# Optimization experiments

Measured on AMD Instinct MI355X. Metric: run time of the kernel, lower is better.

The kernel has to match this reference:

```python
import jax, jax.numpy as jnp
import numpy as np

N = 100000      # nodes
E = 1600000     # edges (avg degree 16)
DIN = 128
DH = 128
DOUT = 64
K = 2           # SGConv propagation steps
EPS = 1e-5      # BatchNorm eps


def setup_inputs() -> dict:
    key = jax.random.key(0)
    ks = jax.random.split(key, 12)
    x = jax.random.normal(ks[0], (N, DIN), dtype=jnp.float32)
    edge_index = jax.random.randint(ks[1], (2, E), 0, N, dtype=jnp.int32)
    def lin(k, fin, fout):
        k1, k2 = jax.random.split(k)
        s = 1.0 / np.sqrt(fin)
        W = jax.random.uniform(k1, (fin, fout), jnp.float32, -s, s)
        b = jax.random.uniform(k2, (fout,), jnp.float32, -s, s)
        return W, b
    W1, b1 = lin(ks[2], DIN, DH)
    W2, b2 = lin(ks[3], DH, DH)
    W3, b3 = lin(ks[4], DH, DOUT)
    g1 = jnp.ones((DH,), jnp.float32); be1 = jnp.zeros((DH,), jnp.float32)
    g2 = jnp.ones((DH,), jnp.float32); be2 = jnp.zeros((DH,), jnp.float32)
    return {"x": x, "edge_index": edge_index,
            "W1": W1, "b1": b1, "g1": g1, "be1": be1,
            "W2": W2, "b2": b2, "g2": g2, "be2": be2,
            "W3": W3, "b3": b3}


def _sgc_propagate(h, row, col, norm):
    # h: [N, d]; gather source nodes, scale per-edge, scatter-add to dest
    for _ in range(K):
        msg = norm[:, None] * h[row]                      # [E, d]
        h = jax.ops.segment_sum(msg, col, num_segments=N)  # [N, d]
    return h


def _batchnorm(h, gamma, beta):
    # training-mode BN over node axis, biased variance (torch semantics)
    mu = jnp.mean(h, axis=0)
    var = jnp.mean(jnp.square(h - mu), axis=0)
    return gamma * (h - mu) * jax.lax.rsqrt(var + EPS) + beta


def reference(x, edge_index, W1, b1, g1, be1, W2, b2, g2, be2, W3, b3):
    row, col = edge_index[0], edge_index[1]
    # symmetric degree normalization; degree counted on row (as in source)
    deg = jax.ops.segment_sum(jnp.ones((E,), x.dtype), row, num_segments=N)
    dis = jnp.where(deg > 0, 1.0 / jnp.sqrt(jnp.maximum(deg, 1.0)), 0.0)
    norm = dis[row] * dis[col]                             # [E]

    h = _sgc_propagate(x, row, col, norm)
    h = _batchnorm(h @ W1 + b1, g1, be1)   # dropout p=0.0 -> identity
    h = _sgc_propagate(h, row, col, norm)
    h = _batchnorm(h @ W2 + b2, g2, be2)
    return h @ W3 + b3                      # [N, DOUT]
```

## Files before the change

kernel.cpp:

```cpp
#include <hip/hip_runtime.h>


typedef __attribute__((ext_vector_type(8))) short bf16x8;
typedef __attribute__((ext_vector_type(4))) float f32x4;

#define HR_RBITS 14
#define HR_RSIZE 16384
#define HR_NRANGE 7
#define HR_NCHUNK 100
#define HR_WPC (HR_NRANGE * HR_RSIZE / 2)

#define PA_NCHUNK 256
#define PB_SHIFT 8

static inline size_t align256(size_t x) { return (x + 255) & ~(size_t)255; }

__device__ inline unsigned short bf16rn(float f) {
    unsigned int u = __builtin_bit_cast(unsigned int, f);
    u += 0x7fffu + ((u >> 16) & 1u);
    return (unsigned short)(u >> 16);
}
__device__ inline float bflo(unsigned int u) { return __builtin_bit_cast(float, u << 16); }
__device__ inline float bfhi(unsigned int u) { return __builtin_bit_cast(float, u & 0xffff0000u); }
__device__ inline unsigned int packbf2(float a, float b) {
    return (unsigned int)bf16rn(a) | ((unsigned int)bf16rn(b) << 16);
}

__global__ void hist_row_kernel(const int* __restrict__ row, int E,
                                unsigned int* __restrict__ staging) {
    __shared__ unsigned int l32[HR_RSIZE / 2];
    int range = blockIdx.x % HR_NRANGE;
    int chunk = blockIdx.x / HR_NRANGE;
    for (int i = threadIdx.x; i < HR_RSIZE / 2; i += 256) l32[i] = 0;
    __syncthreads();
    int lo = range << HR_RBITS;
    int ebeg = (int)((long long)E * chunk / HR_NCHUNK);
    int eend = (int)((long long)E * (chunk + 1) / HR_NCHUNK);
    for (int i = ebeg + threadIdx.x * 4; i + 3 < eend; i += 256 * 4) {
        int4 v = *(const int4*)(row + i);
        unsigned a;
        a = (unsigned)(v.x - lo); if (a < HR_RSIZE) atomicAdd(&l32[a >> 1], (a & 1) ? 0x10000u : 1u);
        a = (unsigned)(v.y - lo); if (a < HR_RSIZE) atomicAdd(&l32[a >> 1], (a & 1) ? 0x10000u : 1u);
        a = (unsigned)(v.z - lo); if (a < HR_RSIZE) atomicAdd(&l32[a >> 1], (a & 1) ? 0x10000u : 1u);
        a = (unsigned)(v.w - lo); if (a < HR_RSIZE) atomicAdd(&l32[a >> 1], (a & 1) ? 0x10000u : 1u);
    }
    __syncthreads();
    unsigned int* dst = staging + (size_t)chunk * HR_WPC + (lo >> 1);
    for (int i = threadIdx.x; i < HR_RSIZE / 2; i += 256) dst[i] = l32[i];
}

__global__ void dis_kernel(const unsigned int* __restrict__ staging, float* __restrict__ dis, int n) {
    int i = blockIdx.x * blockDim.x + threadIdx.x;
    if (i < n) {
        int shift = (i & 1) * 16;
        int d = 0;
#pragma unroll 4
        for (int c = 0; c < HR_NCHUNK; ++c)
            d += (staging[(size_t)c * HR_WPC + (i >> 1)] >> shift) & 0xffff;
        dis[i] = d > 0 ? rsqrtf((float)d) : 0.f;
    }
}


__global__ void pa_hist_kernel(const int* __restrict__ col, int E,
                               int* __restrict__ chunkhist, int nbuck) {
    __shared__ int lh[512];
    int chunk = blockIdx.x;
    for (int i = threadIdx.x; i < nbuck; i += 256) lh[i] = 0;
    __syncthreads();
    int ebeg = (int)((long long)E * chunk / PA_NCHUNK);
    int eend = (int)((long long)E * (chunk + 1) / PA_NCHUNK);
    for (int i = ebeg + threadIdx.x; i < eend; i += 256)
        atomicAdd(&lh[col[i] >> PB_SHIFT], 1);
    __syncthreads();
    for (int i = threadIdx.x; i < nbuck; i += 256)
        chunkhist[i * PA_NCHUNK + chunk] = lh[i];
}

__global__ void pa_scan1_kernel(int* __restrict__ chunkhist, int* __restrict__ tot) {
    __shared__ int sh[PA_NCHUNK];
    int b = blockIdx.x, t = threadIdx.x;
    int* p = chunkhist + b * PA_NCHUNK;
    int v = p[t];
    sh[t] = v;
    __syncthreads();
    for (int off = 1; off < PA_NCHUNK; off <<= 1) {
        int tv = (t >= off) ? sh[t - off] : 0;
        __syncthreads();
        sh[t] += tv;
        __syncthreads();
    }
    p[t] = sh[t] - v;
    if (t == PA_NCHUNK - 1) tot[b] = sh[t];
}

__global__ void pa_scan2_kernel(const int* __restrict__ tot, int* __restrict__ bucketstart,
                                int nbuck) {
    __shared__ int sh[512];
    int t = threadIdx.x;
    int v = (t < nbuck) ? tot[t] : 0;
    sh[t] = v;
    __syncthreads();
    for (int off = 1; off < 512; off <<= 1) {
        int tv = (t >= off) ? sh[t - off] : 0;
        __syncthreads();
        sh[t] += tv;
        __syncthreads();
    }
    if (t < nbuck) bucketstart[t] = sh[t] - v;
    if (t == 511) bucketstart[nbuck] = sh[511];
}

__global__ void pa_scatter_kernel(const int* __restrict__ row, const int* __restrict__ col,
                                  int E, const int* __restrict__ chunkhist,
                                  const int* __restrict__ bucketstart,
                                  int2* __restrict__ part, int nbuck) {
    __shared__ int loff[512];
    int chunk = blockIdx.x;
    for (int i = threadIdx.x; i < nbuck; i += 256)
        loff[i] = chunkhist[i * PA_NCHUNK + chunk] + bucketstart[i];
    __syncthreads();
    int ebeg = (int)((long long)E * chunk / PA_NCHUNK);
    int eend = (int)((long long)E * (chunk + 1) / PA_NCHUNK);
    for (int i = ebeg + threadIdx.x; i < eend; i += 256) {
        int r = row[i], c = col[i];
        int pos = atomicAdd(&loff[c >> PB_SHIFT], 1);
        int2 v; v.x = r; v.y = c;
        part[pos] = v;
    }
}

__global__ void pb_kernel(const int2* __restrict__ part, const int* __restrict__ bucketstart,
                          const float* __restrict__ dis, int2* __restrict__ csr,
                          int* __restrict__ csr_ptr, int n) {
    __shared__ int lcnt[256], sh[256], loff[256];
    int b = blockIdx.x, t = threadIdx.x;
    int nlo = b << PB_SHIFT;
    int ebeg = bucketstart[b], eend = bucketstart[b + 1];
    lcnt[t] = 0;
    __syncthreads();
    for (int i = ebeg + t; i < eend; i += 256)
        atomicAdd(&lcnt[part[i].y - nlo], 1);
    __syncthreads();
    int v = lcnt[t];
    sh[t] = v;
    __syncthreads();
    for (int off = 1; off < 256; off <<= 1) {
        int tv = (t >= off) ? sh[t - off] : 0;
        __syncthreads();
        sh[t] += tv;
        __syncthreads();
    }
    int excl = sh[t] - v;
    loff[t] = excl;
    if (nlo + t <= n) csr_ptr[nlo + t] = ebeg + excl;
    __syncthreads();
    for (int i = ebeg + t; i < eend; i += 256) {
        int2 e = part[i];
        int c = e.y;
        int slot = atomicAdd(&loff[c - nlo], 1);
        int2 o;
        o.x = e.x;
        o.y = __float_as_int(dis[e.x] * dis[c]);
        csr[ebeg + slot] = o;
    }
}


__global__ void xcvt_kernel(const float* __restrict__ x, unsigned int* __restrict__ x16, int total4) {
    for (int i = blockIdx.x * blockDim.x + threadIdx.x; i < total4; i += gridDim.x * blockDim.x) {
        float4 f = ((const float4*)x)[i];
        x16[i * 2] = packbf2(f.x, f.y);
        x16[i * 2 + 1] = packbf2(f.z, f.w);
    }
}

__global__ void wcvt_kernel(const float* __restrict__ W1, const float* __restrict__ W2,
                            unsigned short* __restrict__ W1t, unsigned short* __restrict__ W2t) {
    int i = blockIdx.x * blockDim.x + threadIdx.x;
    if (i < 32768) {
        const float* W = (i < 16384) ? W1 : W2;
        unsigned short* T = (i < 16384) ? W1t : W2t;
        int j = i & 16383;
        int k = j >> 7, c = j & 127;
        T[c * 128 + k] = bf16rn(W[j]);
    }
}


template <bool AFF>
__global__ void spmm16_kernel(const int* __restrict__ csr_ptr, const int2* __restrict__ csr,
                              const unsigned short* __restrict__ h_in,
                              const float* __restrict__ scale, const float* __restrict__ shift,
                              unsigned short* __restrict__ h_out, int n) {
    int gw = __builtin_amdgcn_readfirstlane((blockIdx.x * blockDim.x + threadIdx.x) >> 6);
    int lane = threadIdx.x & 63;
    int sub = lane & 15;
    int grp = lane >> 4;
    if (gw >= n) return;
    uint4* outp = (uint4*)(h_out + (size_t)gw * 128) + sub;
    int beg = csr_ptr[gw];
    int end = csr_ptr[gw + 1];
    int cnt = end - beg;
    if (cnt == 0) {
        if (lane < 16) {
            uint4 z = {0u, 0u, 0u, 0u};
            *outp = z;
        }
        return;
    }
    const int2* base = csr + beg;
    float acc[8];
#pragma unroll
    for (int j = 0; j < 8; ++j) acc[j] = 0.f;
    float sc[8], sh[8];
    if (AFF) {
        float4 s0 = ((const float4*)scale)[sub * 2];
        float4 s1 = ((const float4*)scale)[sub * 2 + 1];
        float4 h0 = ((const float4*)shift)[sub * 2];
        float4 h1 = ((const float4*)shift)[sub * 2 + 1];
        sc[0] = s0.x; sc[1] = s0.y; sc[2] = s0.z; sc[3] = s0.w;
        sc[4] = s1.x; sc[5] = s1.y; sc[6] = s1.z; sc[7] = s1.w;
        sh[0] = h0.x; sh[1] = h0.y; sh[2] = h0.z; sh[3] = h0.w;
        sh[4] = h1.x; sh[5] = h1.y; sh[6] = h1.z; sh[7] = h1.w;
    }
    bool g1 = (grp & 1) != 0;
    bool g2 = (grp & 2) != 0;
    for (int j0 = 0; j0 < cnt; j0 += 16) {
        int2 ent[16];
#pragma unroll
        for (int k = 0; k < 16; ++k) ent[k] = base[j0 + k];
        uint4 u[4];
        float wsel[4];
#pragma unroll
        for (int k = 0; k < 4; ++k) {
            int i0 = j0 + 4 * k;
            int e0 = (i0 + 0 < cnt) ? ent[4 * k + 0].x : 0;
            int e1 = (i0 + 1 < cnt) ? ent[4 * k + 1].x : 0;
            int e2 = (i0 + 2 < cnt) ? ent[4 * k + 2].x : 0;
            int e3 = (i0 + 3 < cnt) ? ent[4 * k + 3].x : 0;
            float w0 = (i0 + 0 < cnt) ? __int_as_float(ent[4 * k + 0].y) : 0.f;
            float w1 = (i0 + 1 < cnt) ? __int_as_float(ent[4 * k + 1].y) : 0.f;
            float w2 = (i0 + 2 < cnt) ? __int_as_float(ent[4 * k + 2].y) : 0.f;
            float w3 = (i0 + 3 < cnt) ? __int_as_float(ent[4 * k + 3].y) : 0.f;
            int eA = g1 ? e1 : e0;
            int eB = g1 ? e3 : e2;
            int esel = g2 ? eB : eA;
            float wA = g1 ? w1 : w0;
            float wB = g1 ? w3 : w2;
            wsel[k] = g2 ? wB : wA;
            u[k] = *(const uint4*)(h_in + (size_t)esel * 128 + sub * 8);
        }
#pragma unroll
        for (int k = 0; k < 4; ++k) {
            float w = wsel[k];
            unsigned int uu[4] = {u[k].x, u[k].y, u[k].z, u[k].w};
#pragma unroll
            for (int q = 0; q < 4; ++q) {
                float f0 = bflo(uu[q]), f1 = bfhi(uu[q]);
                if (AFF) {
                    f0 = fmaf(sc[2 * q], f0, sh[2 * q]);
                    f1 = fmaf(sc[2 * q + 1], f1, sh[2 * q + 1]);
                }
                acc[2 * q] = fmaf(w, f0, acc[2 * q]);
                acc[2 * q + 1] = fmaf(w, f1, acc[2 * q + 1]);
            }
        }
    }
#pragma unroll
    for (int j = 0; j < 8; ++j) {
        acc[j] += __shfl_xor(acc[j], 16, 64);
        acc[j] += __shfl_xor(acc[j], 32, 64);
    }
    if (lane < 16) {
        uint4 o;
        o.x = packbf2(acc[0], acc[1]);
        o.y = packbf2(acc[2], acc[3]);
        o.z = packbf2(acc[4], acc[5]);
        o.w = packbf2(acc[6], acc[7]);
        *outp = o;
    }
}


template <int NCT, bool OUTF32, bool STATS>
__launch_bounds__(256)
__global__ void gemm16_kernel(const unsigned short* __restrict__ X,
                              const unsigned short* __restrict__ Wt,
                              const float* __restrict__ bias, void* __restrict__ Y,
                              float* __restrict__ gsum, float* __restrict__ gsq, int n) {
    __shared__ __align__(16) char lds[NCT * 16 * 256];
    __shared__ float ssum[NCT * 16], ssq[NCT * 16];
    for (int i = threadIdx.x; i < NCT * 16 * 16; i += 256) {
        int col = i >> 4;
        int kbyte = (i & 15) << 4;
        *(uint4*)(lds + col * 256 + (kbyte ^ ((col & 7) << 4))) = ((const uint4*)Wt)[i];
    }
    if (STATS) {
        for (int i = threadIdx.x; i < NCT * 16; i += 256) {
            ssum[i] = 0.f;
            ssq[i] = 0.f;
        }
    }
    __syncthreads();

    int lane = threadIdx.x & 63;
    int wave = threadIdx.x >> 6;
    int cl = lane & 15, g = lane >> 4;

    bf16x8 b[NCT][4];
#pragma unroll
    for (int ct = 0; ct < NCT; ++ct) {
        int col = ct * 16 + cl;
#pragma unroll
        for (int kc = 0; kc < 4; ++kc) {
            int kbyte = kc * 64 + g * 16;
            b[ct][kc] = *(const bf16x8*)(lds + col * 256 + (kbyte ^ ((col & 7) << 4)));
        }
    }
    float bc[NCT];
#pragma unroll
    for (int ct = 0; ct < NCT; ++ct) bc[ct] = bias[ct * 16 + cl];

    for (int rb0 = blockIdx.x * 64; rb0 < n; rb0 += gridDim.x * 64) {
        int rb = rb0 + wave * 16;
        if (rb >= n) continue;
        int row = rb + cl;
        int rowc = row < n ? row : n - 1;
        const unsigned short* xr = X + (size_t)rowc * 128;
        bf16x8 a[4];
#pragma unroll
        for (int kc = 0; kc < 4; ++kc) a[kc] = *(const bf16x8*)(xr + kc * 32 + g * 8);
#pragma unroll
        for (int ct = 0; ct < NCT; ++ct) {
            f32x4 acc = {bc[ct], bc[ct], bc[ct], bc[ct]};
#pragma unroll
            for (int kc = 0; kc < 4; ++kc)
                acc = __builtin_amdgcn_mfma_f32_16x16x32_bf16(a[kc], b[ct][kc], acc, 0, 0, 0);
            int colo = ct * 16 + cl;
            if (STATS) {
                float s = acc[0] + acc[1] + acc[2] + acc[3];
                float q = acc[0] * acc[0] + acc[1] * acc[1] + acc[2] * acc[2] + acc[3] * acc[3];
                s += __shfl_xor(s, 16, 64);
                s += __shfl_xor(s, 32, 64);
                q += __shfl_xor(q, 16, 64);
                q += __shfl_xor(q, 32, 64);
                if (g == 0) {
                    atomicAdd(&ssum[colo], s);
                    atomicAdd(&ssq[colo], q);
                }
            }
#pragma unroll
            for (int i = 0; i < 4; ++i) {
                int ro = rb + g * 4 + i;
                if (ro < n) {
                    if (OUTF32)
                        ((float*)Y)[(size_t)ro * (NCT * 16) + colo] = acc[i];
                    else
                        ((unsigned short*)Y)[(size_t)ro * 128 + colo] = bf16rn(acc[i]);
                }
            }
        }
    }
    if (STATS) {
        __syncthreads();
        for (int i = threadIdx.x; i < NCT * 16; i += 256) {
            atomicAdd(&gsum[i], ssum[i]);
            atomicAdd(&gsq[i], ssq[i]);
        }
    }
}


__global__ void bn_final_kernel(const float* __restrict__ gsum, const float* __restrict__ gsq,
                                const float* __restrict__ gamma, const float* __restrict__ beta,
                                int n, float* __restrict__ scale, float* __restrict__ shift) {
    int c = threadIdx.x;
    if (c < 128) {
        float fn = (float)n;
        float mu = gsum[c] / fn;
        float var = gsq[c] / fn - mu * mu;
        float inv = rsqrtf(var + 1e-5f);
        float sc = gamma[c] * inv;
        scale[c] = sc;
        shift[c] = beta[c] - sc * mu;
    }
}

__global__ void fold_w3_kernel(const float* __restrict__ W3, const float* __restrict__ b3,
                               const float* __restrict__ scale, const float* __restrict__ shift,
                               unsigned short* __restrict__ W3t, float* __restrict__ b3f) {
    int c = threadIdx.x;
    if (c < 64) {
        float acc = b3[c];
        for (int k = 0; k < 128; ++k) {
            float w = W3[k * 64 + c];
            W3t[c * 128 + k] = bf16rn(scale[k] * w);
            acc += shift[k] * w;
        }
        b3f[c] = acc;
    }
}


extern "C" void kernel_launch(void* const* d_in, const int* in_sizes, int n_in,
                              void* d_out, int out_size, void* d_ws, size_t ws_size,
                              hipStream_t stream) {
    const float* x = (const float*)d_in[0];
    const int* edge = (const int*)d_in[1];
    const float* W1 = (const float*)d_in[2];
    const float* b1 = (const float*)d_in[3];
    const float* g1 = (const float*)d_in[4];
    const float* be1 = (const float*)d_in[5];
    const float* W2 = (const float*)d_in[6];
    const float* b2 = (const float*)d_in[7];
    const float* g2 = (const float*)d_in[8];
    const float* be2 = (const float*)d_in[9];
    const float* W3 = (const float*)d_in[10];
    const float* b3 = (const float*)d_in[11];
    float* out = (float*)d_out;

    const int N = in_sizes[0] / 128;
    const int E = in_sizes[1] / 2;
    const int* erow = edge;
    const int* ecol = edge + E;
    const int nbuck = (N + 255) >> PB_SHIFT;

    char* p = (char*)d_ws;
    size_t off = 0;
    auto carve = [&](size_t bytes) {
        void* r = p + off;
        off += align256(bytes);
        return r;
    };
    unsigned short* x16 = (unsigned short*)carve((size_t)N * 128 * 2);
    unsigned short* A16 = (unsigned short*)carve((size_t)N * 128 * 2);
    unsigned short* B16 = (unsigned short*)carve((size_t)N * 128 * 2);
    int2* part = (int2*)carve((size_t)E * 8);
    int2* csr = (int2*)carve((size_t)E * 8 + 256);
    int* csr_ptr = (int*)carve((size_t)(N + 1) * 4);
    int* chunkhist = (int*)carve((size_t)(nbuck + 1) * PA_NCHUNK * 4);
    int* bucketstart = (int*)carve((size_t)(nbuck + 1) * 4);
    int* tot = (int*)carve((size_t)(nbuck + 1) * 4);
    float* dis = (float*)carve((size_t)N * 4);
    float* gsum = (float*)carve(1024);
    float* gsq = (float*)(gsum + 128);
    float* scale1 = (float*)carve(512);
    float* shift1 = (float*)carve(512);
    float* scale2 = (float*)carve(512);
    float* shift2 = (float*)carve(512);
    unsigned short* W1t = (unsigned short*)carve(128 * 128 * 2);
    unsigned short* W2t = (unsigned short*)carve(128 * 128 * 2);
    unsigned short* W3t = (unsigned short*)carve(64 * 128 * 2);
    float* b3f = (float*)carve(256);
    unsigned int* staging = (unsigned int*)part;
    (void)ws_size;

    const int TB = 256;
    const int gN = (N + TB - 1) / TB;
    const int gSp = (N + 3) / 4;
    const int gGemm = (N + 63) / 64;
    const int gGemmS = 320;

    hist_row_kernel<<<HR_NRANGE * HR_NCHUNK, TB, 0, stream>>>(erow, E, staging);
    dis_kernel<<<gN, TB, 0, stream>>>(staging, dis, N);
    pa_hist_kernel<<<PA_NCHUNK, TB, 0, stream>>>(ecol, E, chunkhist, nbuck);
    pa_scan1_kernel<<<nbuck, PA_NCHUNK, 0, stream>>>(chunkhist, tot);
    pa_scan2_kernel<<<1, 512, 0, stream>>>(tot, bucketstart, nbuck);
    pa_scatter_kernel<<<PA_NCHUNK, TB, 0, stream>>>(erow, ecol, E, chunkhist, bucketstart, part, nbuck);
    pb_kernel<<<nbuck, TB, 0, stream>>>(part, bucketstart, dis, csr, csr_ptr, N);

    xcvt_kernel<<<2048, TB, 0, stream>>>(x, (unsigned int*)x16, N * 32);
    wcvt_kernel<<<128, TB, 0, stream>>>(W1, W2, W1t, W2t);

    spmm16_kernel<false><<<gSp, TB, 0, stream>>>(csr_ptr, csr, x16, nullptr, nullptr, A16, N);
    spmm16_kernel<false><<<gSp, TB, 0, stream>>>(csr_ptr, csr, A16, nullptr, nullptr, B16, N);

    hipMemsetAsync(gsum, 0, 1024, stream);
    gemm16_kernel<8, false, true><<<gGemmS, TB, 0, stream>>>(B16, W1t, b1, A16, gsum, gsq, N);
    bn_final_kernel<<<1, 128, 0, stream>>>(gsum, gsq, g1, be1, N, scale1, shift1);

    spmm16_kernel<true><<<gSp, TB, 0, stream>>>(csr_ptr, csr, A16, scale1, shift1, B16, N);
    spmm16_kernel<false><<<gSp, TB, 0, stream>>>(csr_ptr, csr, B16, nullptr, nullptr, A16, N);

    hipMemsetAsync(gsum, 0, 1024, stream);
    gemm16_kernel<8, false, true><<<gGemmS, TB, 0, stream>>>(A16, W2t, b2, B16, gsum, gsq, N);
    bn_final_kernel<<<1, 128, 0, stream>>>(gsum, gsq, g2, be2, N, scale2, shift2);

    fold_w3_kernel<<<1, 64, 0, stream>>>(W3, b3, scale2, shift2, W3t, b3f);
    gemm16_kernel<4, true, false><<<gGemm, TB, 0, stream>>>(B16, W3t, b3f, out, nullptr, nullptr, N);
}
```

Baseline: 400.4 us.

## Switch intermediates to fp16, use dot2 in SpMM and fold BN affine post-aggregation

Intermediate features, weights and edge norms move from bf16 to fp16. The SpMM inner loop now packs two edges' values and weights and uses v_dot2_f32_f16, halving FMA count. The BatchNorm affine is no longer applied per gathered element; it is applied once after aggregation as scale*acc + shift*sum(w). The histogram also gets larger ranges and fewer chunks and now handles a tail of edges. fp16 has less exponent range than bf16, so large intermediate values could overflow.

```diff
diff --git a/kernel.cpp b/kernel.cpp
--- a/kernel.cpp
+++ b/kernel.cpp
@@ -1,13 +1,14 @@
 #include <hip/hip_runtime.h>
-
-
-typedef __attribute__((ext_vector_type(8))) short bf16x8;
+#include <hip/hip_fp16.h>
+
+
+typedef _Float16 f16x8 __attribute__((ext_vector_type(8)));
 typedef __attribute__((ext_vector_type(4))) float f32x4;
 
-#define HR_RBITS 14
-#define HR_RSIZE 16384
-#define HR_NRANGE 7
-#define HR_NCHUNK 100
+#define HR_RBITS 15
+#define HR_RSIZE 32768
+#define HR_NRANGE 4
+#define HR_NCHUNK 96
 #define HR_WPC (HR_NRANGE * HR_RSIZE / 2)
 
 #define PA_NCHUNK 256
@@ -15,15 +16,13 @@
 
 static inline size_t align256(size_t x) { return (x + 255) & ~(size_t)255; }
 
-__device__ inline unsigned short bf16rn(float f) {
-    unsigned int u = __builtin_bit_cast(unsigned int, f);
-    u += 0x7fffu + ((u >> 16) & 1u);
-    return (unsigned short)(u >> 16);
-}
-__device__ inline float bflo(unsigned int u) { return __builtin_bit_cast(float, u << 16); }
-__device__ inline float bfhi(unsigned int u) { return __builtin_bit_cast(float, u & 0xffff0000u); }
-__device__ inline unsigned int packbf2(float a, float b) {
-    return (unsigned int)bf16rn(a) | ((unsigned int)bf16rn(b) << 16);
+__device__ inline unsigned int packh2(float a, float b) {
+    return (unsigned int)__half_as_ushort(__float2half(a)) |
+           ((unsigned int)__half_as_ushort(__float2half(b)) << 16);
+}
+
+__device__ inline void dot2h(float& acc, unsigned int a, unsigned int b) {
+    asm("v_dot2_f32_f16 %0, %1, %2, %0" : "+v"(acc) : "v"(a), "v"(b));
 }
 
 __global__ void hist_row_kernel(const int* __restrict__ row, int E,
@@ -34,8 +33,9 @@
     for (int i = threadIdx.x; i < HR_RSIZE / 2; i += 256) l32[i] = 0;
     __syncthreads();
     int lo = range << HR_RBITS;
-    int ebeg = (int)((long long)E * chunk / HR_NCHUNK);
-    int eend = (int)((long long)E * (chunk + 1) / HR_NCHUNK);
+    int q4 = E >> 2;
+    int ebeg = (int)(((long long)q4 * chunk / HR_NCHUNK) << 2);
+    int eend = (int)(((long long)q4 * (chunk + 1) / HR_NCHUNK) << 2);
     for (int i = ebeg + threadIdx.x * 4; i + 3 < eend; i += 256 * 4) {
         int4 v = *(const int4*)(row + i);
         unsigned a;
@@ -43,6 +43,12 @@
         a = (unsigned)(v.y - lo); if (a < HR_RSIZE) atomicAdd(&l32[a >> 1], (a & 1) ? 0x10000u : 1u);
         a = (unsigned)(v.z - lo); if (a < HR_RSIZE) atomicAdd(&l32[a >> 1], (a & 1) ? 0x10000u : 1u);
         a = (unsigned)(v.w - lo); if (a < HR_RSIZE) atomicAdd(&l32[a >> 1], (a & 1) ? 0x10000u : 1u);
+    }
+    if (chunk == HR_NCHUNK - 1) {
+        for (int i = (E & ~3) + threadIdx.x; i < E; i += 256) {
+            unsigned a = (unsigned)(row[i] - lo);
+            if (a < HR_RSIZE) atomicAdd(&l32[a >> 1], (a & 1) ? 0x10000u : 1u);
+        }
     }
     __syncthreads();
     unsigned int* dst = staging + (size_t)chunk * HR_WPC + (lo >> 1);
@@ -159,9 +165,10 @@
         int2 e = part[i];
         int c = e.y;
         int slot = atomicAdd(&loff[c - nlo], 1);
+        float nrm = dis[e.x] * dis[c];
         int2 o;
         o.x = e.x;
-        o.y = __float_as_int(dis[e.x] * dis[c]);
+        o.y = (int)((unsigned int)__half_as_ushort(__float2half(nrm)) << 16);
         csr[ebeg + slot] = o;
     }
 }
@@ -170,8 +177,8 @@
 __global__ void xcvt_kernel(const float* __restrict__ x, unsigned int* __restrict__ x16, int total4) {
     for (int i = blockIdx.x * blockDim.x + threadIdx.x; i < total4; i += gridDim.x * blockDim.x) {
         float4 f = ((const float4*)x)[i];
-        x16[i * 2] = packbf2(f.x, f.y);
-        x16[i * 2 + 1] = packbf2(f.z, f.w);
+        x16[i * 2] = packh2(f.x, f.y);
+        x16[i * 2 + 1] = packh2(f.z, f.w);
     }
 }
 
@@ -183,7 +190,7 @@
         unsigned short* T = (i < 16384) ? W1t : W2t;
         int j = i & 16383;
         int k = j >> 7, c = j & 127;
-        T[c * 128 + k] = bf16rn(W[j]);
+        T[c * 128 + k] = __half_as_ushort(__float2half(W[j]));
     }
 }
 
@@ -213,17 +220,8 @@
     float acc[8];
 #pragma unroll
     for (int j = 0; j < 8; ++j) acc[j] = 0.f;
-    float sc[8], sh[8];
-    if (AFF) {
-        float4 s0 = ((const float4*)scale)[sub * 2];
-        float4 s1 = ((const float4*)scale)[sub * 2 + 1];
-        float4 h0 = ((const float4*)shift)[sub * 2];
-        float4 h1 = ((const float4*)shift)[sub * 2 + 1];
-        sc[0] = s0.x; sc[1] = s0.y; sc[2] = s0.z; sc[3] = s0.w;
-        sc[4] = s1.x; sc[5] = s1.y; sc[6] = s1.z; sc[7] = s1.w;
-        sh[0] = h0.x; sh[1] = h0.y; sh[2] = h0.z; sh[3] = h0.w;
-        sh[4] = h1.x; sh[5] = h1.y; sh[6] = h1.z; sh[7] = h1.w;
-    }
+    float wsum = 0.f;
+    const unsigned int ones2 = 0x3C003C00u;
     bool g1 = (grp & 1) != 0;
     bool g2 = (grp & 2) != 0;
     for (int j0 = 0; j0 < cnt; j0 += 16) {
@@ -252,18 +250,20 @@
             u[k] = *(const uint4*)(h_in + (size_t)esel * 128 + sub * 8);
         }
 #pragma unroll
-        for (int k = 0; k < 4; ++k) {
-            float w = wsel[k];
-            unsigned int uu[4] = {u[k].x, u[k].y, u[k].z, u[k].w};
+        for (int p = 0; p < 2; ++p) {
+            unsigned int wa = __float_as_uint(wsel[2 * p]);
+            unsigned int wb = __float_as_uint(wsel[2 * p + 1]);
+            unsigned int wp = __builtin_amdgcn_perm(wb, wa, 0x07060302u);
+            if (AFF) dot2h(wsum, ones2, wp);
+            uint4 ua4 = u[2 * p], ub4 = u[2 * p + 1];
+            unsigned int uaw[4] = {ua4.x, ua4.y, ua4.z, ua4.w};
+            unsigned int ubw[4] = {ub4.x, ub4.y, ub4.z, ub4.w};
 #pragma unroll
             for (int q = 0; q < 4; ++q) {
-                float f0 = bflo(uu[q]), f1 = bfhi(uu[q]);
-                if (AFF) {
-                    f0 = fmaf(sc[2 * q], f0, sh[2 * q]);
-                    f1 = fmaf(sc[2 * q + 1], f1, sh[2 * q + 1]);
-                }
-                acc[2 * q] = fmaf(w, f0, acc[2 * q]);
-                acc[2 * q + 1] = fmaf(w, f1, acc[2 * q + 1]);
+                unsigned int lop = __builtin_amdgcn_perm(ubw[q], uaw[q], 0x05040100u);
+                unsigned int hip = __builtin_amdgcn_perm(ubw[q], uaw[q], 0x07060302u);
+                dot2h(acc[2 * q], lop, wp);
+                dot2h(acc[2 * q + 1], hip, wp);
             }
         }
     }
@@ -272,12 +272,28 @@
         acc[j] += __shfl_xor(acc[j], 16, 64);
         acc[j] += __shfl_xor(acc[j], 32, 64);
     }
+    if (AFF) {
+        wsum += __shfl_xor(wsum, 16, 64);
+        wsum += __shfl_xor(wsum, 32, 64);
+        float4 s0 = ((const float4*)scale)[sub * 2];
+        float4 s1 = ((const float4*)scale)[sub * 2 + 1];
+        float4 h0 = ((const float4*)shift)[sub * 2];
+        float4 h1 = ((const float4*)shift)[sub * 2 + 1];
+        acc[0] = fmaf(h0.x, wsum, s0.x * acc[0]);
+        acc[1] = fmaf(h0.y, wsum, s0.y * acc[1]);
+        acc[2] = fmaf(h0.z, wsum, s0.z * acc[2]);
+        acc[3] = fmaf(h0.w, wsum, s0.w * acc[3]);
+        acc[4] = fmaf(h1.x, wsum, s1.x * acc[4]);
+        acc[5] = fmaf(h1.y, wsum, s1.y * acc[5]);
+        acc[6] = fmaf(h1.z, wsum, s1.z * acc[6]);
+        acc[7] = fmaf(h1.w, wsum, s1.w * acc[7]);
+    }
     if (lane < 16) {
         uint4 o;
-        o.x = packbf2(acc[0], acc[1]);
-        o.y = packbf2(acc[2], acc[3]);
-        o.z = packbf2(acc[4], acc[5]);
-        o.w = packbf2(acc[6], acc[7]);
+        o.x = packh2(acc[0], acc[1]);
+        o.y = packh2(acc[2], acc[3]);
+        o.z = packh2(acc[4], acc[5]);
+        o.w = packh2(acc[6], acc[7]);
         *outp = o;
     }
 }
@@ -308,14 +324,14 @@
     int wave = threadIdx.x >> 6;
     int cl = lane & 15, g = lane >> 4;
 
-    bf16x8 b[NCT][4];
+    f16x8 b[NCT][4];
 #pragma unroll
     for (int ct = 0; ct < NCT; ++ct) {
         int col = ct * 16 + cl;
 #pragma unroll
         for (int kc = 0; kc < 4; ++kc) {
             int kbyte = kc * 64 + g * 16;
-            b[ct][kc] = *(const bf16x8*)(lds + col * 256 + (kbyte ^ ((col & 7) << 4)));
+            b[ct][kc] = *(const f16x8*)(lds + col * 256 + (kbyte ^ ((col & 7) << 4)));
         }
     }
     float bc[NCT];
@@ -328,15 +344,15 @@
         int row = rb + cl;
         int rowc = row < n ? row : n - 1;
         const unsigned short* xr = X + (size_t)rowc * 128;
-        bf16x8 a[4];
-#pragma unroll
-        for (int kc = 0; kc < 4; ++kc) a[kc] = *(const bf16x8*)(xr + kc * 32 + g * 8);
+        f16x8 a[4];
+#pragma unroll
+        for (int kc = 0; kc < 4; ++kc) a[kc] = *(const f16x8*)(xr + kc * 32 + g * 8);
 #pragma unroll
         for (int ct = 0; ct < NCT; ++ct) {
             f32x4 acc = {bc[ct], bc[ct], bc[ct], bc[ct]};
 #pragma unroll
             for (int kc = 0; kc < 4; ++kc)
-                acc = __builtin_amdgcn_mfma_f32_16x16x32_bf16(a[kc], b[ct][kc], acc, 0, 0, 0);
+                acc = __builtin_amdgcn_mfma_f32_16x16x32_f16(a[kc], b[ct][kc], acc, 0, 0, 0);
             int colo = ct * 16 + cl;
             if (STATS) {
                 float s = acc[0] + acc[1] + acc[2] + acc[3];
@@ -357,7 +373,8 @@
                     if (OUTF32)
                         ((float*)Y)[(size_t)ro * (NCT * 16) + colo] = acc[i];
                     else
-                        ((unsigned short*)Y)[(size_t)ro * 128 + colo] = bf16rn(acc[i]);
+                        ((unsigned short*)Y)[(size_t)ro * 128 + colo] =
+                            __half_as_ushort(__float2half(acc[i]));
                 }
             }
         }
@@ -395,7 +412,7 @@
         float acc = b3[c];
         for (int k = 0; k < 128; ++k) {
             float w = W3[k * 64 + c];
-            W3t[c * 128 + k] = bf16rn(scale[k] * w);
+            W3t[c * 128 + k] = __half_as_ushort(__float2half(scale[k] * w));
             acc += shift[k] * w;
         }
         b3f[c] = acc;
```

Measured after the change: 396.8 us. Within noise of the previous version (-0.9%).
